# Kernel optimization log

Hardware: AMD Instinct MI355X
Metric: run time of the kernel (lower is better)

## Reference

```python
import jax, jax.numpy as jnp
import numpy as np
from jax import lax

DIM = 384
NH = 8
HD = DIM // NH
M = 16          # num_anchors
B = 16
HH = 64
WW = 64
N = HH * WW
STD = 0.02


def setup_inputs() -> dict:
    key = jax.random.key(0)
    ks = jax.random.split(key, 12)
    rn = lambda k, shape: (jax.random.normal(k, shape, jnp.float32) * STD)
    return {
        "x": jax.random.normal(ks[0], (B, N, DIM), jnp.float32),
        "H": HH,
        "W": WW,
        "saliency_w": rn(ks[1], (DIM, 1)),
        "saliency_b": jnp.zeros((1,), jnp.float32),
        "anchor_seeds": rn(ks[2], (1, M, DIM)),
        "w_q_agg": rn(ks[3], (DIM, DIM)),
        "w_kv_agg": rn(ks[4], (DIM, 2 * DIM)),
        "w_q_self": rn(ks[5], (DIM, DIM)),
        "w_kv_self": rn(ks[6], (DIM, 2 * DIM)),
        "w_q_bcast": rn(ks[7], (DIM, DIM)),
        "w_kv_bcast": rn(ks[8], (DIM, 2 * DIM)),
        "dw_kernel": rn(ks[9], (DIM, 1, 3, 3)),  # depthwise conv, OIHW with I=1
        "w_proj": rn(ks[10], (DIM, DIM)),
    }


def _mhsa(q_in, kv_in, wq, wkv):
    """Multi-head cross attention. q_in: [B,Lq,C], kv_in: [B,Lk,C]."""
    b, lq, c = q_in.shape
    lk = kv_in.shape[1]
    scale = HD ** -0.5
    q = (q_in @ wq).reshape(b, lq, NH, HD)
    kv = (kv_in @ wkv).reshape(b, lk, 2, NH, HD)
    k, v = kv[:, :, 0], kv[:, :, 1]
    attn = jnp.einsum("bqhd,bkhd->bhqk", q, k) * scale
    attn = jax.nn.softmax(attn, axis=-1)
    out = jnp.einsum("bhqk,bkhd->bqhd", attn, v).reshape(b, lq, c)
    return out


def reference(x, H, W, saliency_w, saliency_b, anchor_seeds,
              w_q_agg, w_kv_agg, w_q_self, w_kv_self,
              w_q_bcast, w_kv_bcast, dw_kernel, w_proj):
    b, n, c = x.shape
    # saliency gating
    sal = jax.nn.sigmoid(x @ saliency_w + saliency_b)  # [B,N,1]
    x_sal = x * sal
    # stage 1: anchors aggregate from saliency-gated tokens
    anchors = jnp.broadcast_to(anchor_seeds, (b, M, c))
    anchors = anchors + _mhsa(anchors, x_sal, w_q_agg, w_kv_agg)
    # stage 2: anchor self-attention
    anchors = anchors + _mhsa(anchors, anchors, w_q_self, w_kv_self)
    # stage 3: broadcast anchors back to all tokens
    global_out = _mhsa(x, anchors, w_q_bcast, w_kv_bcast)
    # depthwise 3x3 conv on the 2D token map
    x2d = x.reshape(b, H, W, c).transpose(0, 3, 1, 2)  # NCHW
    local = lax.conv_general_dilated(
        x2d, dw_kernel, window_strides=(1, 1), padding="SAME",
        feature_group_count=c,
        dimension_numbers=("NCHW", "OIHW", "NCHW"))
    local = local.transpose(0, 2, 3, 1).reshape(b, n, c)
    return (global_out + local) @ w_proj
```

## Files before the change

### kernel.cpp

```cpp
#include <hip/hip_runtime.h>
#include <hip/hip_bf16.h>

#define SCALE 0.14433756729740643f

typedef __attribute__((ext_vector_type(8))) short bf16x8;
typedef __attribute__((ext_vector_type(4))) float f32x4;

template <typename T> __device__ inline T cvt_from_f(float v);
template <> __device__ inline float cvt_from_f<float>(float v) { return v; }
template <> __device__ inline __hip_bfloat16 cvt_from_f<__hip_bfloat16>(float v) { return __float2bfloat16(v); }

__device__ inline void gload16(const void* g, void* l) {
  __builtin_amdgcn_global_load_lds((const __attribute__((address_space(1))) void*)g,
                                   (__attribute__((address_space(3))) void*)l, 16, 0, 0);
}

__device__ inline int xcd_flat(int nwg) {
  int flat = (blockIdx.z * gridDim.y + blockIdx.y) * gridDim.x + blockIdx.x;
  int per = nwg >> 3;
  return (flat & 7) * per + (flat >> 3);
}

__global__ __launch_bounds__(256) void prep(const float* __restrict__ x,
                                            const float* __restrict__ wsal,
                                            const float* __restrict__ bsal,
                                            __hip_bfloat16* __restrict__ xb,
                                            float* __restrict__ sal) {
  int wave = threadIdx.x >> 6, lane = threadIdx.x & 63;
  size_t row = (size_t)blockIdx.x * 4 + wave;
  const float* xr = x + row * 384;
  float xs[6];
  float part = 0.f;
#pragma unroll
  for (int j = 0; j < 6; j++) {
    int c = lane + 64 * j;
    xs[j] = xr[c];
    part += xs[j] * wsal[c];
  }
#pragma unroll
  for (int off = 32; off >= 1; off >>= 1) part += __shfl_xor(part, off);
  float s = 1.f / (1.f + __expf(-(part + bsal[0])));
#pragma unroll
  for (int j = 0; j < 6; j++) {
    int c = lane + 64 * j;
    xb[row * 384 + c] = __float2bfloat16(xs[j]);
  }
  if (lane == 0) sal[row] = s;
}

__global__ void wcast_tv(const float* __restrict__ w, __hip_bfloat16* __restrict__ wt) {
  int idx = blockIdx.x * 256 + threadIdx.x;
  if (idx >= 384 * 384) return;
  int n = idx / 384, k = idx % 384;
  wt[idx] = __float2bfloat16(w[(size_t)k * 768 + 384 + n]);
}

template <int K, typename OT, int BSHIFT>
__global__ __launch_bounds__(256) void gemm_mfma(const __hip_bfloat16* __restrict__ A,
                                                 const __hip_bfloat16* __restrict__ BT,
                                                 OT* __restrict__ out, int Ncols,
                                                 size_t btBatchStride) {
  __shared__ __align__(16) __hip_bfloat16 Asl[128][32];
  __shared__ __align__(16) __hip_bfloat16 Bsl[128][32];
  int nf = xcd_flat(gridDim.x * gridDim.y);
  int bX = nf % gridDim.x, bY = nf / gridDim.x;
  int tid = threadIdx.x;
  int lane = tid & 63;
  int w = tid >> 6;
  int wr = w >> 1, wc = w & 1;
  int fr = lane & 15, fq = lane >> 4;
  int rowBase = bY * 128, colBase = bX * 128;
  const __hip_bfloat16* BTb = BT + (size_t)(rowBase >> BSHIFT) * btBatchStride;

  int r1 = tid >> 2, kc1 = tid & 3;
  int r2 = (tid + 256) >> 2;

  char* aB1 = (char*)Asl + (size_t)(w * 64) * 16;
  char* aB2 = (char*)Asl + (size_t)(256 + w * 64) * 16;
  char* bB1 = (char*)Bsl + (size_t)(w * 64) * 16;
  char* bB2 = (char*)Bsl + (size_t)(256 + w * 64) * 16;

  const __hip_bfloat16* a1 = A + (size_t)(rowBase + r1) * K + kc1 * 8;
  const __hip_bfloat16* a2 = A + (size_t)(rowBase + r2) * K + kc1 * 8;
  const __hip_bfloat16* b1 = BTb + (size_t)(colBase + r1) * K + kc1 * 8;
  const __hip_bfloat16* b2 = BTb + (size_t)(colBase + r2) * K + kc1 * 8;

  f32x4 acc[4][4] = {};

  for (int kk = 0; kk < K; kk += 32) {
    gload16(a1 + kk, aB1);
    gload16(a2 + kk, aB2);
    gload16(b1 + kk, bB1);
    gload16(b2 + kk, bB2);
    __syncthreads();
    bf16x8 af[4], bfv[4];
#pragma unroll
    for (int m = 0; m < 4; m++) af[m] = *(const bf16x8*)&Asl[wr * 64 + m * 16 + fr][fq * 8];
#pragma unroll
    for (int n = 0; n < 4; n++) bfv[n] = *(const bf16x8*)&Bsl[wc * 64 + n * 16 + fr][fq * 8];
#pragma unroll
    for (int m = 0; m < 4; m++)
#pragma unroll
      for (int n = 0; n < 4; n++)
        acc[m][n] = __builtin_amdgcn_mfma_f32_16x16x32_bf16(af[m], bfv[n], acc[m][n], 0, 0, 0);
    __syncthreads();
  }

#pragma unroll
  for (int m = 0; m < 4; m++) {
    int row0 = rowBase + wr * 64 + m * 16 + fq * 4;
#pragma unroll
    for (int n = 0; n < 4; n++) {
      int col = colBase + wc * 64 + n * 16 + fr;
      f32x4 v = acc[m][n];
#pragma unroll
      for (int r = 0; r < 4; r++) out[(size_t)(row0 + r) * Ncols + col] = cvt_from_f<OT>(v[r]);
    }
  }
}

__global__ __launch_bounds__(256) void gemm_vlog(const __hip_bfloat16* __restrict__ A,
                                                 const __hip_bfloat16* __restrict__ BT,
                                                 __hip_bfloat16* __restrict__ vT,
                                                 __hip_bfloat16* __restrict__ lgT,
                                                 const float* __restrict__ rowScale) {
  constexpr int K = 384;
  __shared__ __align__(16) __hip_bfloat16 Asl[128][32];
  __shared__ __align__(16) __hip_bfloat16 Bsl[128][32];
  int nf = xcd_flat(2048);
  int bX = nf & 3, bY = nf >> 2;
  int tid = threadIdx.x;
  int lane = tid & 63;
  int w = tid >> 6;
  int wr = w >> 1, wc = w & 1;
  int fr = lane & 15, fq = lane >> 4;
  int rowBase = bY * 128, colBase = bX * 128;

  int r1 = tid >> 2, kc1 = tid & 3;
  int r2 = (tid + 256) >> 2;

  char* aB1 = (char*)Asl + (size_t)(w * 64) * 16;
  char* aB2 = (char*)Asl + (size_t)(256 + w * 64) * 16;
  char* bB1 = (char*)Bsl + (size_t)(w * 64) * 16;
  char* bB2 = (char*)Bsl + (size_t)(256 + w * 64) * 16;

  const __hip_bfloat16* a1 = A + (size_t)(rowBase + r1) * K + kc1 * 8;
  const __hip_bfloat16* a2 = A + (size_t)(rowBase + r2) * K + kc1 * 8;
  const __hip_bfloat16* b1 = BT + (size_t)(colBase + r1) * K + kc1 * 8;
  const __hip_bfloat16* b2 = BT + (size_t)(colBase + r2) * K + kc1 * 8;

  f32x4 acc[4][4] = {};

  for (int kk = 0; kk < K; kk += 32) {
    gload16(a1 + kk, aB1);
    gload16(a2 + kk, aB2);
    gload16(b1 + kk, bB1);
    gload16(b2 + kk, bB2);
    __syncthreads();
    bf16x8 af[4], bfv[4];
#pragma unroll
    for (int m = 0; m < 4; m++) af[m] = *(const bf16x8*)&Asl[wr * 64 + m * 16 + fr][fq * 8];
#pragma unroll
    for (int n = 0; n < 4; n++) bfv[n] = *(const bf16x8*)&Bsl[wc * 64 + n * 16 + fr][fq * 8];
#pragma unroll
    for (int m = 0; m < 4; m++)
#pragma unroll
      for (int n = 0; n < 4; n++)
        acc[m][n] = __builtin_amdgcn_mfma_f32_16x16x32_bf16(af[m], bfv[n], acc[m][n], 0, 0, 0);
    __syncthreads();
  }

  float sv[4][4];
#pragma unroll
  for (int m = 0; m < 4; m++)
#pragma unroll
    for (int r = 0; r < 4; r++)
      sv[m][r] = rowScale[rowBase + wr * 64 + m * 16 + fq * 4 + r];

  if (bX < 3) {
#pragma unroll
    for (int m = 0; m < 4; m++) {
      int row0 = rowBase + wr * 64 + m * 16 + fq * 4;
      int bb = row0 >> 12;
      int n0 = row0 & 4095;
#pragma unroll
      for (int n = 0; n < 4; n++) {
        int col = colBase + wc * 64 + n * 16 + fr;
        __hip_bfloat16 tb[4];
#pragma unroll
        for (int r = 0; r < 4; r++) tb[r] = __float2bfloat16(acc[m][n][r] * sv[m][r]);
        *(unsigned long long*)(vT + ((size_t)bb * 384 + col) * 4096 + n0) = *(unsigned long long*)tb;
      }
    }
  } else {
#pragma unroll
    for (int m = 0; m < 4; m++) {
      int row0 = rowBase + wr * 64 + m * 16 + fq * 4;
      int bb = row0 >> 12;
      int n0 = row0 & 4095;
#pragma unroll
      for (int n = 0; n < 4; n++) {
        int col = wc * 64 + n * 16 + fr;
        __hip_bfloat16 tb[4];
#pragma unroll
        for (int r = 0; r < 4; r++) tb[r] = __float2bfloat16(acc[m][n][r] * sv[m][r]);
        *(unsigned long long*)(lgT + ((size_t)bb * 128 + col) * 4096 + n0) = *(unsigned long long*)tb;
      }
    }
  }
}

__global__ __launch_bounds__(256) void gemm_pv(const __hip_bfloat16* __restrict__ PT,
                                               const __hip_bfloat16* __restrict__ vT,
                                               float* __restrict__ pbuf) {
  __shared__ __align__(16) __hip_bfloat16 Asl[128][32];
  __shared__ __align__(16) __hip_bfloat16 Bsl[128][32];
  int nf = xcd_flat(384);
  int bX = nf % 3, bY = (nf / 3) & 15, kz = nf / 48;
  int tid = threadIdx.x;
  int lane = tid & 63;
  int w = tid >> 6;
  int wr = w >> 1, wc = w & 1;
  int fr = lane & 15, fq = lane >> 4;
  int rowBase = bY * 128, colBase = bX * 128;
  const __hip_bfloat16* BTb = vT + (size_t)bY * 384 * 4096;

  int r1 = tid >> 2, kc1 = tid & 3;
  int r2 = (tid + 256) >> 2;

  char* aB1 = (char*)Asl + (size_t)(w * 64) * 16;
  char* aB2 = (char*)Asl + (size_t)(256 + w * 64) * 16;
  char* bB1 = (char*)Bsl + (size_t)(w * 64) * 16;
  char* bB2 = (char*)Bsl + (size_t)(256 + w * 64) * 16;

  const __hip_bfloat16* a1 = PT + (size_t)(rowBase + r1) * 4096 + kz * 512 + kc1 * 8;
  const __hip_bfloat16* a2 = PT + (size_t)(rowBase + r2) * 4096 + kz * 512 + kc1 * 8;
  const __hip_bfloat16* b1 = BTb + (size_t)(colBase + r1) * 4096 + kz * 512 + kc1 * 8;
  const __hip_bfloat16* b2 = BTb + (size_t)(colBase + r2) * 4096 + kz * 512 + kc1 * 8;

  f32x4 acc[4][4] = {};

  for (int kk = 0; kk < 512; kk += 32) {
    gload16(a1 + kk, aB1);
    gload16(a2 + kk, aB2);
    gload16(b1 + kk, bB1);
    gload16(b2 + kk, bB2);
    __syncthreads();
    bf16x8 af[4], bfv[4];
#pragma unroll
    for (int m = 0; m < 4; m++) af[m] = *(const bf16x8*)&Asl[wr * 64 + m * 16 + fr][fq * 8];
#pragma unroll
    for (int n = 0; n < 4; n++) bfv[n] = *(const bf16x8*)&Bsl[wc * 64 + n * 16 + fr][fq * 8];
#pragma unroll
    for (int m = 0; m < 4; m++)
#pragma unroll
      for (int n = 0; n < 4; n++)
        acc[m][n] = __builtin_amdgcn_mfma_f32_16x16x32_bf16(af[m], bfv[n], acc[m][n], 0, 0, 0);
    __syncthreads();
  }

  float* outz = pbuf + (size_t)kz * 786432;
#pragma unroll
  for (int m = 0; m < 4; m++) {
    int row0 = rowBase + wr * 64 + m * 16 + fq * 4;
#pragma unroll
    for (int n = 0; n < 4; n++) {
      int col = colBase + wc * 64 + n * 16 + fr;
      f32x4 v = acc[m][n];
#pragma unroll
      for (int r = 0; r < 4; r++) outz[(size_t)(row0 + r) * 384 + col] = v[r];
    }
  }
}

__global__ void anch_fix2(const float* __restrict__ pbuf, const float* __restrict__ seeds,
                          float* __restrict__ anch1) {
  int idx = blockIdx.x * 256 + threadIdx.x;
  int b = idx / 6144;
  int rem = idx - b * 6144;
  int m = rem / 384, c = rem - m * 384;
  int g = b * 128 + (c / 48) * 16 + m;
  const float* p = pbuf + (size_t)g * 384 + c;
  float s = 0.f;
#pragma unroll
  for (int z = 0; z < 8; z++) s += p[(size_t)z * 786432];
  anch1[idx] = seeds[rem] + s;
}

__global__ __launch_bounds__(256) void softmax_rows(const __hip_bfloat16* __restrict__ lgT,
                                                    __hip_bfloat16* __restrict__ PT) {
  int g = blockIdx.x;
  const __hip_bfloat16* row = lgT + (size_t)g * 4096;
  int tid = threadIdx.x, wv = tid >> 6, lane = tid & 63;
  __shared__ float redm[4], reds[4];
  float v[16];
  union { ulonglong2 u; __hip_bfloat16 h[8]; } L0, L1;
  L0.u = *(const ulonglong2*)(row + tid * 16);
  L1.u = *(const ulonglong2*)(row + tid * 16 + 8);
#pragma unroll
  for (int i = 0; i < 8; i++) {
    v[i] = __bfloat162float(L0.h[i]);
    v[8 + i] = __bfloat162float(L1.h[i]);
  }
  float mx = v[0];
#pragma unroll
  for (int i = 1; i < 16; i++) mx = fmaxf(mx, v[i]);
#pragma unroll
  for (int off = 1; off < 64; off <<= 1) mx = fmaxf(mx, __shfl_xor(mx, off));
  if (lane == 0) redm[wv] = mx;
  __syncthreads();
  mx = fmaxf(fmaxf(redm[0], redm[1]), fmaxf(redm[2], redm[3]));
  float s = 0.f;
#pragma unroll
  for (int i = 0; i < 16; i++) {
    v[i] = __expf(v[i] - mx);
    s += v[i];
  }
#pragma unroll
  for (int off = 1; off < 64; off <<= 1) s += __shfl_xor(s, off);
  if (lane == 0) reds[wv] = s;
  __syncthreads();
  s = (reds[0] + reds[1]) + (reds[2] + reds[3]);
  float inv = 1.f / s;
  __hip_bfloat16 tb[16];
#pragma unroll
  for (int i = 0; i < 16; i++) tb[i] = __float2bfloat16(v[i] * inv);
  __hip_bfloat16* op = PT + (size_t)g * 4096 + tid * 16;
  *(ulonglong2*)op = *(ulonglong2*)tb;
  *(ulonglong2*)(op + 8) = *(ulonglong2*)(tb + 8);
}

__global__ void fill_wl(const float* __restrict__ wkv, const float* __restrict__ qseed,
                        __hip_bfloat16* __restrict__ wvlT) {
  int idx = blockIdx.x * 256 + threadIdx.x;
  int hm = idx / 384, ci = idx - hm * 384;
  int h = hm >> 4, m = hm & 15;
  const float* wp = wkv + (size_t)ci * 768 + h * 48;
  const float* qp = qseed + m * 384 + h * 48;
  float acc = 0.f;
#pragma unroll
  for (int d = 0; d < 48; d++) acc += wp[d] * qp[d];
  wvlT[384 * 384 + idx] = __float2bfloat16(acc);
}

__global__ __launch_bounds__(256) void wtrans(const float* __restrict__ wproj,
                                              __hip_bfloat16* __restrict__ bt2) {
  __shared__ float t[64][65];
  int kt = blockIdx.x * 64, ct = blockIdx.y * 64;
  int tid = threadIdx.x;
  int c = tid & 63, r4 = tid >> 6;
#pragma unroll
  for (int i = 0; i < 16; i++) {
    int r = i * 4 + r4;
    t[r][c] = wproj[(size_t)(kt + r) * 384 + ct + c];
  }
  __syncthreads();
  __hip_bfloat16 vals[16];
#pragma unroll
  for (int i = 0; i < 16; i++) vals[i] = __float2bfloat16(t[c][i * 4 + r4]);
  for (int b = blockIdx.z * 4; b < blockIdx.z * 4 + 4; b++) {
    __hip_bfloat16* dst = bt2 + (size_t)b * 196608;
#pragma unroll
    for (int i = 0; i < 16; i++) {
      int rr = i * 4 + r4;
      dst[(size_t)(ct + rr) * 512 + kt + c] = vals[i];
    }
  }
}

__global__ __launch_bounds__(256) void fill_wv2(const float* __restrict__ wproj,
                                                const float* __restrict__ kvb,
                                                __hip_bfloat16* __restrict__ bt2) {
  int h = blockIdx.x, b = blockIdx.y;
  __shared__ float vbs[16][48];
  int tid = threadIdx.x;
  for (int idx = tid; idx < 768; idx += 256) {
    int m = idx / 48, d = idx % 48;
    vbs[m][d] = kvb[(size_t)(b * 16 + m) * 768 + 384 + h * 48 + d];
  }
  __syncthreads();
  for (int cp = tid; cp < 384; cp += 256) {
    float acc[16] = {};
    for (int d = 0; d < 48; d++) {
      float wv = wproj[(size_t)(h * 48 + d) * 384 + cp];
#pragma unroll
      for (int m = 0; m < 16; m++) acc[m] += vbs[m][d] * wv;
    }
    __hip_bfloat16 tb[16];
#pragma unroll
    for (int m = 0; m < 16; m++) tb[m] = __float2bfloat16(acc[m]);
    __hip_bfloat16* dst = bt2 + (size_t)b * 196608 + (size_t)cp * 512 + 384 + h * 16;
    *(ulonglong2*)dst = *(ulonglong2*)tb;
    *(ulonglong2*)(dst + 8) = *(ulonglong2*)(tb + 8);
  }
}

__global__ __launch_bounds__(256) void fill_wpb2(const float* __restrict__ wq,
                                                 const float* __restrict__ kvb,
                                                 __hip_bfloat16* __restrict__ wpbT) {
  int h = blockIdx.x, b = blockIdx.y;
  __shared__ float kbs[16][48];
  __shared__ __hip_bfloat16 obuf[16][264];
  int tid = threadIdx.x;
  for (int idx = tid; idx < 768; idx += 256) {
    int m = idx / 48, d = idx % 48;
    kbs[m][d] = kvb[(size_t)(b * 16 + m) * 768 + h * 48 + d];
  }
  __syncthreads();
  for (int kbase = 0; kbase < 384; kbase += 256) {
    int chunk = (kbase == 0) ? 256 : 128;
    if (tid < chunk) {
      int k = kbase + tid;
      const float4* wp = (const float4*)(wq + (size_t)k * 384 + h * 48);
      float acc[16] = {};
#pragma unroll
      for (int dq = 0; dq < 12; dq++) {
        float4 wv = wp[dq];
#pragma unroll
        for (int m = 0; m < 16; m++)
          acc[m] += kbs[m][dq * 4] * wv.x + kbs[m][dq * 4 + 1] * wv.y +
                    kbs[m][dq * 4 + 2] * wv.z + kbs[m][dq * 4 + 3] * wv.w;
      }
#pragma unroll
      for (int m = 0; m < 16; m++) obuf[m][tid] = __float2bfloat16(acc[m]);
    }
    __syncthreads();
    for (int widx = tid; widx < 16 * chunk; widx += 256) {
      int m = widx / chunk, kk = widx - m * chunk;
      wpbT[(size_t)b * 49152 + (size_t)(h * 16 + m) * 384 + kbase + kk] = obuf[m][kk];
    }
    __syncthreads();
  }
}

__global__ __launch_bounds__(256) void pgemm_conv(const __hip_bfloat16* __restrict__ A,
                                                  const __hip_bfloat16* __restrict__ wpbT,
                                                  const float* __restrict__ dwk,
                                                  __hip_bfloat16* __restrict__ A2) {
  constexpr int K = 384;
  __shared__ __align__(16) __hip_bfloat16 Asl[128][32];
  __shared__ __align__(16) __hip_bfloat16 Bsl[128][32];
  int tid = threadIdx.x;
  int lane = tid & 63;
  int w = tid >> 6;
  int wr = w >> 1, wc = w & 1;
  int fr = lane & 15, fq = lane >> 4;
  int rowBase = blockIdx.y * 128;
  const __hip_bfloat16* BTb = wpbT + (size_t)(rowBase >> 12) * (128 * 384);

  int r1 = tid >> 2, kc1 = tid & 3;
  int r2 = (tid + 256) >> 2;

  char* aB1 = (char*)Asl + (size_t)(w * 64) * 16;
  char* aB2 = (char*)Asl + (size_t)(256 + w * 64) * 16;
  char* bB1 = (char*)Bsl + (size_t)(w * 64) * 16;
  char* bB2 = (char*)Bsl + (size_t)(256 + w * 64) * 16;

  const __hip_bfloat16* a1 = A + (size_t)(rowBase + r1) * K + kc1 * 8;
  const __hip_bfloat16* a2 = A + (size_t)(rowBase + r2) * K + kc1 * 8;
  const __hip_bfloat16* b1 = BTb + (size_t)r1 * K + kc1 * 8;
  const __hip_bfloat16* b2 = BTb + (size_t)r2 * K + kc1 * 8;

  f32x4 acc[4][4] = {};

  for (int kk = 0; kk < K; kk += 32) {
    gload16(a1 + kk, aB1);
    gload16(a2 + kk, aB2);
    gload16(b1 + kk, bB1);
    gload16(b2 + kk, bB2);
    __syncthreads();
    bf16x8 af[4], bfv[4];
#pragma unroll
    for (int m = 0; m < 4; m++) af[m] = *(const bf16x8*)&Asl[wr * 64 + m * 16 + fr][fq * 8];
#pragma unroll
    for (int n = 0; n < 4; n++) bfv[n] = *(const bf16x8*)&Bsl[wc * 64 + n * 16 + fr][fq * 8];
#pragma unroll
    for (int m = 0; m < 4; m++)
#pragma unroll
      for (int n = 0; n < 4; n++)
        acc[m][n] = __builtin_amdgcn_mfma_f32_16x16x32_bf16(af[m], bfv[n], acc[m][n], 0, 0, 0);
    __syncthreads();
  }

#pragma unroll
  for (int m = 0; m < 4; m++) {
    int row0 = rowBase + wr * 64 + m * 16 + fq * 4;
#pragma unroll
    for (int n = 0; n < 4; n++) {
      int col = wc * 64 + n * 16 + fr;
      f32x4 v = acc[m][n];
      f32x4 mx = v;
#pragma unroll
      for (int off = 1; off < 16; off <<= 1)
#pragma unroll
        for (int r = 0; r < 4; r++) mx[r] = fmaxf(mx[r], __shfl_xor(mx[r], off));
      f32x4 e;
#pragma unroll
      for (int r = 0; r < 4; r++) e[r] = __expf(v[r] - mx[r]);
      f32x4 s = e;
#pragma unroll
      for (int off = 1; off < 16; off <<= 1)
#pragma unroll
        for (int r = 0; r < 4; r++) s[r] += __shfl_xor(s[r], off);
#pragma unroll
      for (int r = 0; r < 4; r++)
        A2[(size_t)(row0 + r) * 512 + 384 + col] = __float2bfloat16(e[r] / s[r]);
    }
  }

  int c0 = lane * 6;
  float kw[6][9];
#pragma unroll
  for (int i = 0; i < 6; i++)
#pragma unroll
    for (int ki = 0; ki < 9; ki++) kw[i][ki] = dwk[(c0 + i) * 9 + ki];
  int bb2 = rowBase >> 12;
  int p0 = rowBase & 4095;
  for (int it = 0; it < 32; it++) {
    int p = p0 + w * 32 + it;
    int y = p >> 6, wx = p & 63;
    size_t prow = (size_t)rowBase + w * 32 + it;
    float acc2[6] = {};
#pragma unroll
    for (int dy = -1; dy <= 1; dy++) {
      int yy = y + dy;
      if (yy < 0 || yy >= 64) continue;
#pragma unroll
      for (int dx = -1; dx <= 1; dx++) {
        int ww2 = wx + dx;
        if (ww2 < 0 || ww2 >= 64) continue;
        int ki = (dy + 1) * 3 + (dx + 1);
        const __hip_bfloat16* xp = A + ((size_t)(bb2 * 4096 + yy * 64 + ww2)) * 384 + c0;
#pragma unroll
        for (int i = 0; i < 6; i++) acc2[i] += __bfloat162float(xp[i]) * kw[i][ki];
      }
    }
    __hip_bfloat16 tb[6];
#pragma unroll
    for (int i = 0; i < 6; i++) tb[i] = __float2bfloat16(acc2[i]);
    __hip_bfloat16* gp = A2 + prow * 512 + c0;
    *(unsigned int*)(gp) = *(unsigned int*)(tb);
    *(unsigned int*)(gp + 2) = *(unsigned int*)(tb + 2);
    *(unsigned int*)(gp + 4) = *(unsigned int*)(tb + 4);
  }
}

__global__ __launch_bounds__(256) void anchor_proj2(const float* __restrict__ A,
                                                    const float* __restrict__ W,
                                                    float* __restrict__ out, int wstride,
                                                    int scaleCols) {
  int cs = blockIdx.x * 16;
  int b = blockIdx.y;
  __shared__ float a1[16][385];
  int tid = threadIdx.x;
  for (int idx = tid; idx < 6144; idx += 256) a1[idx / 384][idx % 384] = A[b * 6144 + idx];
  __syncthreads();
  int m = tid >> 4, cc = tid & 15;
  int col = cs + cc;
  const float* wp = W + col;
  float acc0 = 0.f, acc1 = 0.f, acc2 = 0.f, acc3 = 0.f;
#pragma unroll 4
  for (int k = 0; k < 384; k += 4) {
    acc0 += a1[m][k] * wp[(size_t)k * wstride];
    acc1 += a1[m][k + 1] * wp[(size_t)(k + 1) * wstride];
    acc2 += a1[m][k + 2] * wp[(size_t)(k + 2) * wstride];
    acc3 += a1[m][k + 3] * wp[(size_t)(k + 3) * wstride];
  }
  float acc = (acc0 + acc1) + (acc2 + acc3);
  if (col < scaleCols) acc *= SCALE;
  out[((size_t)b * 16 + m) * wstride + col] = acc;
}

__global__ __launch_bounds__(256) void anchor_proj_qkv(const float* __restrict__ A,
                                                       const float* __restrict__ Wq,
                                                       const float* __restrict__ Wkv,
                                                       float* __restrict__ q_out,
                                                       float* __restrict__ kv_out) {
  bool isQ = blockIdx.x < 24;
  int bx = isQ ? blockIdx.x : blockIdx.x - 24;
  const float* W = isQ ? Wq : Wkv;
  float* outp = isQ ? q_out : kv_out;
  int wstride = isQ ? 384 : 768;
  float scale = isQ ? SCALE : 1.f;
  int cs = bx * 16;
  int b = blockIdx.y;
  __shared__ float a1[16][385];
  int tid = threadIdx.x;
  for (int idx = tid; idx < 6144; idx += 256) a1[idx / 384][idx % 384] = A[b * 6144 + idx];
  __syncthreads();
  int m = tid >> 4, cc = tid & 15;
  int col = cs + cc;
  const float* wp = W + col;
  float acc0 = 0.f, acc1 = 0.f, acc2 = 0.f, acc3 = 0.f;
#pragma unroll 4
  for (int k = 0; k < 384; k += 4) {
    acc0 += a1[m][k] * wp[(size_t)k * wstride];
    acc1 += a1[m][k + 1] * wp[(size_t)(k + 1) * wstride];
    acc2 += a1[m][k + 2] * wp[(size_t)(k + 2) * wstride];
    acc3 += a1[m][k + 3] * wp[(size_t)(k + 3) * wstride];
  }
  float acc = ((acc0 + acc1) + (acc2 + acc3)) * scale;
  outp[((size_t)b * 16 + m) * wstride + col] = acc;
}

__global__ void self_attn(const float* __restrict__ qsf, const float* __restrict__ kvs,
                          const float* __restrict__ anch1, float* __restrict__ anch2) {
  int h = blockIdx.x & 7, b = blockIdx.x >> 3;
  __shared__ float qs[16][48], ks[16][48], vs[16][48], p[16][17];
  int tid = threadIdx.x;
  for (int idx = tid; idx < 768; idx += 256) {
    int m = idx / 48, d = idx % 48;
    qs[m][d] = qsf[(b * 16 + m) * 384 + h * 48 + d];
    ks[m][d] = kvs[(b * 16 + m) * 768 + h * 48 + d];
    vs[m][d] = kvs[(b * 16 + m) * 768 + 384 + h * 48 + d];
  }
  __syncthreads();
  {
    int mq = tid >> 4, mk = tid & 15;
    float acc = 0.f;
    for (int d = 0; d < 48; d++) acc += qs[mq][d] * ks[mk][d];
    p[mq][mk] = acc;
  }
  __syncthreads();
  if (tid < 16) {
    float mx = -1e30f;
    for (int mk = 0; mk < 16; mk++) mx = fmaxf(mx, p[tid][mk]);
    float sum = 0.f;
    for (int mk = 0; mk < 16; mk++) {
      float e = __expf(p[tid][mk] - mx);
      p[tid][mk] = e;
      sum += e;
    }
    float inv = 1.f / sum;
    for (int mk = 0; mk < 16; mk++) p[tid][mk] *= inv;
  }
  __syncthreads();
  for (int idx = tid; idx < 768; idx += 256) {
    int m = idx / 48, d = idx % 48;
    float acc = 0.f;
    for (int mk = 0; mk < 16; mk++) acc += p[m][mk] * vs[mk][d];
    int c = h * 48 + d;
    anch2[(b * 16 + m) * 384 + c] = anch1[(b * 16 + m) * 384 + c] + acc;
  }
}

extern "C" void kernel_launch(void* const* d_in, const int* in_sizes, int n_in,
                              void* d_out, int out_size, void* d_ws, size_t ws_size,
                              hipStream_t stream) {
  (void)in_sizes; (void)n_in; (void)out_size; (void)ws_size;
  const float* x = (const float*)d_in[0];
  const float* wsal = (const float*)d_in[3];
  const float* bsal = (const float*)d_in[4];
  const float* seeds = (const float*)d_in[5];
  const float* w_q_agg = (const float*)d_in[6];
  const float* w_kv_agg = (const float*)d_in[7];
  const float* w_q_self = (const float*)d_in[8];
  const float* w_kv_self = (const float*)d_in[9];
  const float* w_q_bcast = (const float*)d_in[10];
  const float* w_kv_bcast = (const float*)d_in[11];
  const float* dwk = (const float*)d_in[12];
  const float* w_proj = (const float*)d_in[13];
  float* out = (float*)d_out;

  char* ws = (char*)d_ws;
  size_t off = 0;
  auto take = [&](size_t bytes) -> void* {
    void* p = ws + off;
    off += (bytes + 255) & ~(size_t)255;
    return p;
  };
  __hip_bfloat16* xb = (__hip_bfloat16*)take(50331648);
  __hip_bfloat16* vT = (__hip_bfloat16*)take(50331648);
  char* lgRegion = (char*)take(33554432);
  __hip_bfloat16* PT = (__hip_bfloat16*)take(16777216);
  float* qseed = (float*)take(24576);
  float* sal = (float*)take(262144);
  float* anch1 = (float*)take(393216);
  float* anch2 = (float*)take(393216);
  float* q_self = (float*)take(393216);
  float* kv_self = (float*)take(786432);
  float* kv_b = (float*)take(786432);
  __hip_bfloat16* wvlT = (__hip_bfloat16*)take(393216);
  __hip_bfloat16* wpbT = (__hip_bfloat16*)take(1572864);
  __hip_bfloat16* bt2 = (__hip_bfloat16*)take(6291456);
  __hip_bfloat16* logitsT = (__hip_bfloat16*)lgRegion;
  float* pbuf = (float*)lgRegion;
  __hip_bfloat16* A2 = vT;

  prep<<<16384, 256, 0, stream>>>(x, wsal, bsal, xb, sal);
  anchor_proj2<<<dim3(24, 1), 256, 0, stream>>>(seeds, w_q_agg, qseed, 384, 384);
  wcast_tv<<<576, 256, 0, stream>>>(w_kv_agg, wvlT);
  fill_wl<<<192, 256, 0, stream>>>(w_kv_agg, qseed, wvlT);
  wtrans<<<dim3(6, 6, 4), 256, 0, stream>>>(w_proj, bt2);
  gemm_vlog<<<dim3(4, 512), 256, 0, stream>>>(xb, wvlT, vT, logitsT, sal);
  softmax_rows<<<2048, 256, 0, stream>>>(logitsT, PT);
  gemm_pv<<<dim3(3, 16, 8), 256, 0, stream>>>(PT, vT, pbuf);
  anch_fix2<<<384, 256, 0, stream>>>(pbuf, seeds, anch1);
  anchor_proj_qkv<<<dim3(72, 16), 256, 0, stream>>>(anch1, w_q_self, w_kv_self, q_self, kv_self);
  self_attn<<<128, 256, 0, stream>>>(q_self, kv_self, anch1, anch2);
  anchor_proj2<<<dim3(48, 16), 256, 0, stream>>>(anch2, w_kv_bcast, kv_b, 768, 384);
  fill_wpb2<<<dim3(8, 16), 256, 0, stream>>>(w_q_bcast, kv_b, wpbT);
  fill_wv2<<<dim3(8, 16), 256, 0, stream>>>(w_proj, kv_b, bt2);
  pgemm_conv<<<dim3(1, 512), 256, 0, stream>>>(xb, wpbT, dwk, A2);
  gemm_mfma<512, float, 12><<<dim3(3, 512), 256, 0, stream>>>(A2, bt2, out, 384, (size_t)384 * 512);
}
```

Measured before the change: 352.9 us.

## Split depthwise conv into sliding-window kernel and merge fold-weight kernels

Merges the two small per-batch weight folding kernels into one launch with 16x16 blocks, and splits the depthwise 3x3 convolution out of the logits GEMM into its own kernel. The new conv kernel gives each block one image row and each wave a 16-pixel strip, sliding a register window of three columns so each input column is loaded once instead of up to nine times. This removes a launch and redundant conv loads, but adds a separate kernel launch and the conv no longer overlaps with the GEMM tail.

```diff
diff --git a/kernel.cpp b/kernel.cpp
--- a/kernel.cpp
+++ b/kernel.cpp
@@ -368,75 +368,73 @@
   }
 }
 
-__global__ __launch_bounds__(256) void fill_wv2(const float* __restrict__ wproj,
-                                                const float* __restrict__ kvb,
-                                                __hip_bfloat16* __restrict__ bt2) {
-  int h = blockIdx.x, b = blockIdx.y;
-  __shared__ float vbs[16][48];
-  int tid = threadIdx.x;
-  for (int idx = tid; idx < 768; idx += 256) {
-    int m = idx / 48, d = idx % 48;
-    vbs[m][d] = kvb[(size_t)(b * 16 + m) * 768 + 384 + h * 48 + d];
-  }
-  __syncthreads();
-  for (int cp = tid; cp < 384; cp += 256) {
-    float acc[16] = {};
-    for (int d = 0; d < 48; d++) {
-      float wv = wproj[(size_t)(h * 48 + d) * 384 + cp];
-#pragma unroll
-      for (int m = 0; m < 16; m++) acc[m] += vbs[m][d] * wv;
-    }
-    __hip_bfloat16 tb[16];
-#pragma unroll
-    for (int m = 0; m < 16; m++) tb[m] = __float2bfloat16(acc[m]);
-    __hip_bfloat16* dst = bt2 + (size_t)b * 196608 + (size_t)cp * 512 + 384 + h * 16;
-    *(ulonglong2*)dst = *(ulonglong2*)tb;
-    *(ulonglong2*)(dst + 8) = *(ulonglong2*)(tb + 8);
-  }
-}
-
-__global__ __launch_bounds__(256) void fill_wpb2(const float* __restrict__ wq,
+__global__ __launch_bounds__(256) void fill_fold(const float* __restrict__ wq,
+                                                 const float* __restrict__ wproj,
                                                  const float* __restrict__ kvb,
-                                                 __hip_bfloat16* __restrict__ wpbT) {
-  int h = blockIdx.x, b = blockIdx.y;
-  __shared__ float kbs[16][48];
+                                                 __hip_bfloat16* __restrict__ wpbT,
+                                                 __hip_bfloat16* __restrict__ bt2) {
+  int b = blockIdx.y;
+  int tid = threadIdx.x;
+  __shared__ float stage[16][48];
   __shared__ __hip_bfloat16 obuf[16][264];
-  int tid = threadIdx.x;
-  for (int idx = tid; idx < 768; idx += 256) {
-    int m = idx / 48, d = idx % 48;
-    kbs[m][d] = kvb[(size_t)(b * 16 + m) * 768 + h * 48 + d];
-  }
-  __syncthreads();
-  for (int kbase = 0; kbase < 384; kbase += 256) {
-    int chunk = (kbase == 0) ? 256 : 128;
-    if (tid < chunk) {
-      int k = kbase + tid;
-      const float4* wp = (const float4*)(wq + (size_t)k * 384 + h * 48);
+  if (blockIdx.x < 8) {
+    int h = blockIdx.x;
+    for (int idx = tid; idx < 768; idx += 256) {
+      int m = idx / 48, d = idx % 48;
+      stage[m][d] = kvb[(size_t)(b * 16 + m) * 768 + h * 48 + d];
+    }
+    __syncthreads();
+    for (int kbase = 0; kbase < 384; kbase += 256) {
+      int chunk = (kbase == 0) ? 256 : 128;
+      if (tid < chunk) {
+        int k = kbase + tid;
+        const float4* wp = (const float4*)(wq + (size_t)k * 384 + h * 48);
+        float acc[16] = {};
+#pragma unroll
+        for (int dq = 0; dq < 12; dq++) {
+          float4 wv = wp[dq];
+#pragma unroll
+          for (int m = 0; m < 16; m++)
+            acc[m] += stage[m][dq * 4] * wv.x + stage[m][dq * 4 + 1] * wv.y +
+                      stage[m][dq * 4 + 2] * wv.z + stage[m][dq * 4 + 3] * wv.w;
+        }
+#pragma unroll
+        for (int m = 0; m < 16; m++) obuf[m][tid] = __float2bfloat16(acc[m]);
+      }
+      __syncthreads();
+      for (int widx = tid; widx < 16 * chunk; widx += 256) {
+        int m = widx / chunk, kk = widx - m * chunk;
+        wpbT[(size_t)b * 49152 + (size_t)(h * 16 + m) * 384 + kbase + kk] = obuf[m][kk];
+      }
+      __syncthreads();
+    }
+  } else {
+    int h = blockIdx.x - 8;
+    for (int idx = tid; idx < 768; idx += 256) {
+      int m = idx / 48, d = idx % 48;
+      stage[m][d] = kvb[(size_t)(b * 16 + m) * 768 + 384 + h * 48 + d];
+    }
+    __syncthreads();
+    for (int cp = tid; cp < 384; cp += 256) {
       float acc[16] = {};
-#pragma unroll
-      for (int dq = 0; dq < 12; dq++) {
-        float4 wv = wp[dq];
-#pragma unroll
-        for (int m = 0; m < 16; m++)
-          acc[m] += kbs[m][dq * 4] * wv.x + kbs[m][dq * 4 + 1] * wv.y +
-                    kbs[m][dq * 4 + 2] * wv.z + kbs[m][dq * 4 + 3] * wv.w;
+      for (int d = 0; d < 48; d++) {
+        float wv = wproj[(size_t)(h * 48 + d) * 384 + cp];
+#pragma unroll
+        for (int m = 0; m < 16; m++) acc[m] += stage[m][d] * wv;
       }
-#pragma unroll
-      for (int m = 0; m < 16; m++) obuf[m][tid] = __float2bfloat16(acc[m]);
-    }
-    __syncthreads();
-    for (int widx = tid; widx < 16 * chunk; widx += 256) {
-      int m = widx / chunk, kk = widx - m * chunk;
-      wpbT[(size_t)b * 49152 + (size_t)(h * 16 + m) * 384 + kbase + kk] = obuf[m][kk];
-    }
-    __syncthreads();
-  }
-}
-
-__global__ __launch_bounds__(256) void pgemm_conv(const __hip_bfloat16* __restrict__ A,
-                                                  const __hip_bfloat16* __restrict__ wpbT,
-                                                  const float* __restrict__ dwk,
-                                                  __hip_bfloat16* __restrict__ A2) {
+      __hip_bfloat16 tb[16];
+#pragma unroll
+      for (int m = 0; m < 16; m++) tb[m] = __float2bfloat16(acc[m]);
+      __hip_bfloat16* dst = bt2 + (size_t)b * 196608 + (size_t)cp * 512 + 384 + h * 16;
+      *(ulonglong2*)dst = *(ulonglong2*)tb;
+      *(ulonglong2*)(dst + 8) = *(ulonglong2*)(tb + 8);
+    }
+  }
+}
+
+__global__ __launch_bounds__(256) void pgemm(const __hip_bfloat16* __restrict__ A,
+                                             const __hip_bfloat16* __restrict__ wpbT,
+                                             __hip_bfloat16* __restrict__ A2) {
   constexpr int K = 384;
   __shared__ __align__(16) __hip_bfloat16 Asl[128][32];
   __shared__ __align__(16) __hip_bfloat16 Bsl[128][32];
@@ -507,41 +505,89 @@
         A2[(size_t)(row0 + r) * 512 + 384 + col] = __float2bfloat16(e[r] / s[r]);
     }
   }
-
+}
+
+__global__ __launch_bounds__(256) void dwconv3(const __hip_bfloat16* __restrict__ xb,
+                                               const float* __restrict__ dwk,
+                                               __hip_bfloat16* __restrict__ A2) {
+  int b = blockIdx.y;
+  int y = blockIdx.x;
+  int w = threadIdx.x >> 6, lane = threadIdx.x & 63;
   int c0 = lane * 6;
-  float kw[6][9];
-#pragma unroll
-  for (int i = 0; i < 6; i++)
-#pragma unroll
-    for (int ki = 0; ki < 9; ki++) kw[i][ki] = dwk[(c0 + i) * 9 + ki];
-  int bb2 = rowBase >> 12;
-  int p0 = rowBase & 4095;
-  for (int it = 0; it < 32; it++) {
-    int p = p0 + w * 32 + it;
-    int y = p >> 6, wx = p & 63;
-    size_t prow = (size_t)rowBase + w * 32 + it;
-    float acc2[6] = {};
-#pragma unroll
-    for (int dy = -1; dy <= 1; dy++) {
-      int yy = y + dy;
-      if (yy < 0 || yy >= 64) continue;
-#pragma unroll
-      for (int dx = -1; dx <= 1; dx++) {
-        int ww2 = wx + dx;
-        if (ww2 < 0 || ww2 >= 64) continue;
-        int ki = (dy + 1) * 3 + (dx + 1);
-        const __hip_bfloat16* xp = A + ((size_t)(bb2 * 4096 + yy * 64 + ww2)) * 384 + c0;
-#pragma unroll
-        for (int i = 0; i < 6; i++) acc2[i] += __bfloat162float(xp[i]) * kw[i][ki];
+  int x0 = w * 16;
+  float kw[9][6];
+#pragma unroll
+  for (int ki = 0; ki < 9; ki++)
+#pragma unroll
+    for (int i = 0; i < 6; i++) kw[ki][i] = dwk[(c0 + i) * 9 + ki];
+
+  const __hip_bfloat16* base = xb + ((size_t)(b * 4096 + y * 64)) * 384 + c0;
+  bool yv[3];
+#pragma unroll
+  for (int t = 0; t < 3; t++) {
+    int yy = y + t - 1;
+    yv[t] = (yy >= 0 && yy < 64);
+  }
+
+  float colL[3][6], colC[3][6], colR[3][6];
+  auto loadcol = [&](float (&dst)[3][6], int x) {
+#pragma unroll
+    for (int t = 0; t < 3; t++) {
+      if (yv[t]) {
+        const __hip_bfloat16* p = base + ((size_t)(t - 1) * 64 + x) * 384;
+#pragma unroll
+        for (int i = 0; i < 6; i++) dst[t][i] = __bfloat162float(p[i]);
+      } else {
+#pragma unroll
+        for (int i = 0; i < 6; i++) dst[t][i] = 0.f;
       }
     }
+  };
+
+  if (x0 == 0) {
+#pragma unroll
+    for (int t = 0; t < 3; t++)
+#pragma unroll
+      for (int i = 0; i < 6; i++) colL[t][i] = 0.f;
+  } else {
+    loadcol(colL, x0 - 1);
+  }
+  loadcol(colC, x0);
+
+  for (int step = 0; step < 16; step++) {
+    int x = x0 + step;
+    if (x + 1 < 64) {
+      loadcol(colR, x + 1);
+    } else {
+#pragma unroll
+      for (int t = 0; t < 3; t++)
+#pragma unroll
+        for (int i = 0; i < 6; i++) colR[t][i] = 0.f;
+    }
+    float acc[6];
+#pragma unroll
+    for (int i = 0; i < 6; i++) {
+      float a = 0.f;
+#pragma unroll
+      for (int t = 0; t < 3; t++)
+        a += colL[t][i] * kw[t * 3 + 0][i] + colC[t][i] * kw[t * 3 + 1][i] +
+             colR[t][i] * kw[t * 3 + 2][i];
+      acc[i] = a;
+    }
     __hip_bfloat16 tb[6];
 #pragma unroll
-    for (int i = 0; i < 6; i++) tb[i] = __float2bfloat16(acc2[i]);
-    __hip_bfloat16* gp = A2 + prow * 512 + c0;
+    for (int i = 0; i < 6; i++) tb[i] = __float2bfloat16(acc[i]);
+    __hip_bfloat16* gp = A2 + ((size_t)(b * 4096 + y * 64 + x)) * 512 + c0;
     *(unsigned int*)(gp) = *(unsigned int*)(tb);
     *(unsigned int*)(gp + 2) = *(unsigned int*)(tb + 2);
     *(unsigned int*)(gp + 4) = *(unsigned int*)(tb + 4);
+#pragma unroll
+    for (int t = 0; t < 3; t++)
+#pragma unroll
+      for (int i = 0; i < 6; i++) {
+        colL[t][i] = colC[t][i];
+        colC[t][i] = colR[t][i];
+      }
   }
 }
 
@@ -699,8 +745,8 @@
   anchor_proj_qkv<<<dim3(72, 16), 256, 0, stream>>>(anch1, w_q_self, w_kv_self, q_self, kv_self);
   self_attn<<<128, 256, 0, stream>>>(q_self, kv_self, anch1, anch2);
   anchor_proj2<<<dim3(48, 16), 256, 0, stream>>>(anch2, w_kv_bcast, kv_b, 768, 384);
-  fill_wpb2<<<dim3(8, 16), 256, 0, stream>>>(w_q_bcast, kv_b, wpbT);
-  fill_wv2<<<dim3(8, 16), 256, 0, stream>>>(w_proj, kv_b, bt2);
-  pgemm_conv<<<dim3(1, 512), 256, 0, stream>>>(xb, wpbT, dwk, A2);
+  fill_fold<<<dim3(16, 16), 256, 0, stream>>>(w_q_bcast, w_proj, kv_b, wpbT, bt2);
+  pgemm<<<dim3(1, 512), 256, 0, stream>>>(xb, wpbT, A2);
+  dwconv3<<<dim3(64, 16), 256, 0, stream>>>(xb, dwk, A2);
   gemm_mfma<512, float, 12><<<dim3(3, 512), 256, 0, stream>>>(A2, bt2, out, 384, (size_t)384 * 512);
 }
```

After: 345.3 us. 1.02x faster.
